# Kernel tuning notes

Measured on AMD Instinct MI355X. Metric: run time of the kernel, lower is better.

## Reference

```python
import jax, jax.numpy as jnp
import numpy as np

ENTRY_SIZE = 8192
TUPLE_SIZE = 16
N_NEURONS = ENTRY_SIZE // TUPLE_SIZE            # 512
ADDR_SPACE = 2 ** TUPLE_SIZE                     # 65536
BATCH = 4096


def setup_inputs() -> dict:
    key = jax.random.key(0)
    k1, k2, k3 = jax.random.split(key, 3)
    # Binary input bits [B, entry_size]
    inp = jax.random.randint(k1, (BATCH, ENTRY_SIZE), 0, 2, dtype=jnp.int32)
    # Permutation mapping bits -> tuples (identity permutation; arange fill)
    tuple_mapping = jnp.arange(ENTRY_SIZE, dtype=jnp.int64)
    # Dense RAM tables emulating the per-neuron dicts:
    #   counts[n, a] = number of training samples that hit address a in neuron n
    #                  (0 means the address was never trained -> not in dict)
    #   sums[n, a]   = accumulated target sum for that address
    counts = jax.random.randint(k2, (N_NEURONS, ADDR_SPACE), 0, 4, dtype=jnp.int32)
    sums = jax.random.normal(k3, (N_NEURONS, ADDR_SPACE), dtype=jnp.float32)
    return {"input": inp, "tuple_mapping": tuple_mapping, "counts": counts, "sums": sums}


def reference(input, tuple_mapping, counts, sums):
    """RegressionWisard.predict with centrality='mean'.

    input:  [B, entry_size] binary bits (int32)
    tuple_mapping: [entry_size] permutation (int)
    counts: [n_neurons, 2^tuple_size] int32 RAM hit counts
    sums:   [n_neurons, 2^tuple_size] float32 RAM target sums
    """
    B = input.shape[0]
    # Map and group bits into tuples: [B, N, T]
    mapped = jnp.take(input, tuple_mapping, axis=1).reshape(B, N_NEURONS, TUPLE_SIZE)
    # Binary address per (sample, neuron); tidx flips so bit 0 is the MSB.
    pow2 = (jnp.int32(1) << jnp.arange(TUPLE_SIZE - 1, -1, -1, dtype=jnp.int32))
    addr = jnp.einsum("bnt,t->bn", mapped, pow2)  # [B, N], values in [0, 2^T)
    neuron_idx = jnp.arange(N_NEURONS, dtype=jnp.int32)[None, :]  # [1, N]
    c = counts[neuron_idx, addr]  # [B, N]
    s = sums[neuron_idx, addr]    # [B, N]
    trained = c > 0               # dict-membership (torch.isin) equivalent
    response = jnp.sum(jnp.where(trained, s, jnp.float32(0)), axis=1)      # [B]
    counters = jnp.sum(jnp.where(trained, c, 0), axis=1).astype(s.dtype)   # [B]
    return jnp.nan_to_num(response / counters)
```

## Files before the change

kernel.cpp:

```cpp
#include <hip/hip_runtime.h>


constexpr int BATCH   = 4096;
constexpr int ENTRY   = 8192;
constexpr int TUP     = 16;
constexpr int NEUR    = ENTRY / TUP;
constexpr int LINES   = 4096;
constexpr int THREADS = 256;

typedef int v4i __attribute__((ext_vector_type(4)));

__device__ __forceinline__ int tuple_addr(
    const int* __restrict__ input, const int* __restrict__ map_n,
    int m0, bool contig, int s)
{
    if (contig) {
        const v4i* p = reinterpret_cast<const v4i*>(input + (size_t)s * ENTRY + m0);
        const v4i a0 = __builtin_nontemporal_load(p);
        const v4i a1 = __builtin_nontemporal_load(p + 1);
        const v4i a2 = __builtin_nontemporal_load(p + 2);
        const v4i a3 = __builtin_nontemporal_load(p + 3);
        return ((a0.x & 1) << 15) | ((a0.y & 1) << 14)
             | ((a0.z & 1) << 13) | ((a0.w & 1) << 12)
             | ((a1.x & 1) << 11) | ((a1.y & 1) << 10)
             | ((a1.z & 1) <<  9) | ((a1.w & 1) <<  8)
             | ((a2.x & 1) <<  7) | ((a2.y & 1) <<  6)
             | ((a2.z & 1) <<  5) | ((a2.w & 1) <<  4)
             | ((a3.x & 1) <<  3) | ((a3.y & 1) <<  2)
             | ((a3.z & 1) <<  1) |  (a3.w & 1);
    } else {
        const int* row = input + (size_t)s * ENTRY;
        int a = 0;
        #pragma unroll
        for (int t = 0; t < TUP; ++t) a = (a << 1) | (row[map_n[t]] & 1);
        return a;
    }
}

__device__ __forceinline__ int sel4(v4i v, int e01) {
    const int ab = (e01 & 1) ? v.y : v.x;
    const int cd = (e01 & 1) ? v.w : v.z;
    return (e01 & 2) ? cd : ab;
}
__device__ __forceinline__ int sel16(v4i v0, v4i v1, v4i v2, v4i v3, int e) {
    const int e2 = e & 3;
    const int a = sel4(v0, e2), b = sel4(v1, e2);
    const int c = sel4(v2, e2), d = sel4(v3, e2);
    const int ab = (e & 4) ? b : a;
    const int cd = (e & 4) ? d : c;
    return (e & 8) ? cd : ab;
}

__global__ __launch_bounds__(THREADS) void wisard_addr(
    const int* __restrict__ input,
    const int* __restrict__ mapping,
    unsigned short* __restrict__ addr_t)
{
    const int lane = threadIdx.x & 63;
    const int w    = threadIdx.x >> 6;
    const int s    = blockIdx.x * 4 + w;

    #pragma unroll 2
    for (int j = 0; j < NEUR / 64; ++j) {
        const int n = j * 64 + lane;
        const int* map_n = mapping + n * TUP;
        const int m0 = map_n[0];
        bool contig = ((m0 & 3) == 0);
        #pragma unroll
        for (int t = 1; t < TUP; ++t) contig &= (map_n[t] == m0 + t);
        const int a = tuple_addr(input, map_n, m0, contig, s);
        addr_t[(size_t)s * NEUR + n] = (unsigned short)a;
    }
}

__global__ __launch_bounds__(THREADS) void wisard_stream(
    const unsigned short* __restrict__ addr_t,
    const int*   __restrict__ counts,
    const float* __restrict__ sums,
    float2*      __restrict__ contrib)
{
    __shared__ unsigned int hist[LINES];
    __shared__ unsigned int sorted[BATCH];
    __shared__ float2 acc[BATCH];

    const int tid  = threadIdx.x;
    const int lane = tid & 63;
    const int w    = tid >> 6;
    const int n = (blockIdx.x & 7) * 64 + (blockIdx.x >> 3);

    unsigned int a[16];
    #pragma unroll
    for (int j = 0; j < 16; ++j)
        a[j] = addr_t[(size_t)(j * THREADS + tid) * NEUR + n];

    #pragma unroll
    for (int j = 0; j < LINES / THREADS; ++j) hist[j * THREADS + tid] = 0u;
    __syncthreads();
    #pragma unroll
    for (int j = 0; j < 16; ++j) atomicAdd(&hist[a[j] >> 4], 1u);
    __syncthreads();

    unsigned int* ttot = reinterpret_cast<unsigned int*>(acc);
    unsigned int* wsum = ttot + THREADS;
    unsigned int loc[16];
    unsigned int run = 0;
    #pragma unroll
    for (int j = 0; j < 16; ++j) { loc[j] = run; run += hist[tid * 16 + j]; }
    ttot[tid] = run;
    __syncthreads();
    unsigned int v = ttot[tid];
    #pragma unroll
    for (int off = 1; off < 64; off <<= 1) {
        const unsigned int u = __shfl_up(v, off, 64);
        if (lane >= off) v += u;
    }
    if (lane == 63) wsum[w] = v;
    __syncthreads();
    unsigned int woff = 0;
    for (int i = 0; i < w; ++i) woff += wsum[i];
    const unsigned int excl = woff + v - run;
    #pragma unroll
    for (int j = 0; j < 16; ++j) hist[tid * 16 + j] = excl + loc[j];
    __syncthreads();

    #pragma unroll
    for (int j = 0; j < 16; ++j) {
        const unsigned int pos = atomicAdd(&hist[a[j] >> 4], 1u);
        sorted[pos] = (a[j] << 12) | (unsigned int)(j * THREADS + tid);
    }
    __syncthreads();

    #pragma unroll
    for (int j = 0; j < 16; ++j) acc[j * THREADS + tid] = make_float2(0.0f, 0.0f);
    __syncthreads();

    const size_t tbase = (size_t)n << 16;
    for (int j = 0; j < 16; ++j) {
        const int L = j * THREADS + tid;
        const v4i* cp = reinterpret_cast<const v4i*>(counts + tbase + ((size_t)L << 4));
        const v4i* sp = reinterpret_cast<const v4i*>(
            reinterpret_cast<const int*>(sums) + tbase + ((size_t)L << 4));
        const v4i c0 = __builtin_nontemporal_load(cp);
        const v4i c1 = __builtin_nontemporal_load(cp + 1);
        const v4i c2 = __builtin_nontemporal_load(cp + 2);
        const v4i c3 = __builtin_nontemporal_load(cp + 3);
        const v4i s0 = __builtin_nontemporal_load(sp);
        const v4i s1 = __builtin_nontemporal_load(sp + 1);
        const v4i s2 = __builtin_nontemporal_load(sp + 2);
        const v4i s3 = __builtin_nontemporal_load(sp + 3);
        const unsigned int beg = (L == 0) ? 0u : hist[L - 1];
        const unsigned int end = hist[L];
        for (unsigned int k = beg; k < end; ++k) {
            const unsigned int pk = sorted[k];
            const int e  = (int)((pk >> 12) & 15u);
            const int sm = (int)(pk & 4095u);
            const int cv = sel16(c0, c1, c2, c3, e);
            const int sb = sel16(s0, s1, s2, s3, e);
            if (cv > 0) {
                float2 o;
                o.x = __int_as_float(sb);
                o.y = __int_as_float(cv);
                acc[sm] = o;
            }
        }
    }
    __syncthreads();

    #pragma unroll
    for (int j = 0; j < 16; ++j) {
        const int s = j * THREADS + tid;
        contrib[(size_t)n * BATCH + s] = acc[s];
    }
}

__global__ __launch_bounds__(THREADS) void wisard_final(
    const float2* __restrict__ contrib,
    float*        __restrict__ out)
{
    __shared__ float sr [4][64];
    __shared__ int   scn[4][64];
    const int tid  = threadIdx.x;
    const int lane = tid & 63;
    const int w    = tid >> 6;
    const int s    = blockIdx.x * 64 + lane;

    float r = 0.0f; int c = 0;
    #pragma unroll 8
    for (int i = 0; i < NEUR / 4; ++i) {
        const int n = w * (NEUR / 4) + i;
        const float2 vv = contrib[(size_t)n * BATCH + s];
        r += vv.x;
        c += __float_as_int(vv.y);
    }
    sr[w][lane] = r; scn[w][lane] = c;
    __syncthreads();
    if (w == 0) {
        r = sr[0][lane] + sr[1][lane] + sr[2][lane] + sr[3][lane];
        c = scn[0][lane] + scn[1][lane] + scn[2][lane] + scn[3][lane];
        out[s] = (c > 0) ? (r / (float)c) : 0.0f;
    }
}

__global__ __launch_bounds__(THREADS) void wisard_fallback(
    const int*   __restrict__ input,
    const int*   __restrict__ mapping,
    const int*   __restrict__ counts,
    const float* __restrict__ sums,
    float*       __restrict__ out)
{
    __shared__ float s_resp[2][THREADS / 64];
    __shared__ int   s_cnt [2][THREADS / 64];

    const int tid  = threadIdx.x;
    const int lane = tid & 63;
    const int wv   = tid >> 6;
    const int b0   = blockIdx.x * 2;

    int   cv[2][2];
    float sv[2][2];

    #pragma unroll
    for (int k = 0; k < 2; ++k) {
        const int n = tid + k * THREADS;
        const int* map_n = mapping + n * TUP;
        const int m0 = map_n[0];
        bool contig = ((m0 & 3) == 0);
        #pragma unroll
        for (int t = 1; t < TUP; ++t) contig &= (map_n[t] == m0 + t);
        #pragma unroll
        for (int s = 0; s < 2; ++s) {
            const int a = tuple_addr(input, map_n, m0, contig, b0 + s);
            const size_t idx = ((size_t)n << 16) | (unsigned)a;
            cv[s][k] = counts[idx];
            sv[s][k] = sums[idx];
        }
    }

    float resp[2]; int cnt[2];
    #pragma unroll
    for (int s = 0; s < 2; ++s) {
        resp[s] = 0.0f; cnt[s] = 0;
        #pragma unroll
        for (int k = 0; k < 2; ++k) {
            const bool t = cv[s][k] > 0;
            resp[s] += t ? sv[s][k] : 0.0f;
            cnt [s] += t ? cv[s][k] : 0;
        }
    }
    #pragma unroll
    for (int s = 0; s < 2; ++s) {
        float r = resp[s]; int c = cnt[s];
        #pragma unroll
        for (int off = 32; off > 0; off >>= 1) {
            r += __shfl_down(r, off, 64);
            c += __shfl_down(c, off, 64);
        }
        if (lane == 0) { s_resp[s][wv] = r; s_cnt[s][wv] = c; }
    }
    __syncthreads();
    if (tid < 2) {
        float r = 0.0f; int c = 0;
        #pragma unroll
        for (int w = 0; w < THREADS / 64; ++w) { r += s_resp[tid][w]; c += s_cnt[tid][w]; }
        out[b0 + tid] = (c > 0) ? (r / (float)c) : 0.0f;
    }
}

extern "C" void kernel_launch(void* const* d_in, const int* in_sizes, int n_in,
                              void* d_out, int out_size, void* d_ws, size_t ws_size,
                              hipStream_t stream) {
    (void)in_sizes; (void)n_in; (void)out_size;
    const int*   input   = (const int*)d_in[0];
    const int*   mapping = (const int*)d_in[1];
    const int*   counts  = (const int*)d_in[2];
    const float* sums    = (const float*)d_in[3];
    float*       out     = (float*)d_out;

    const size_t contrib_bytes = (size_t)NEUR * BATCH * sizeof(float2);
    const size_t addr_bytes    = (size_t)BATCH * NEUR * sizeof(unsigned short);

    if (ws_size < contrib_bytes + addr_bytes || d_ws == nullptr) {
        wisard_fallback<<<BATCH / 2, THREADS, 0, stream>>>(
            input, mapping, counts, sums, out);
        return;
    }

    float2*         contrib = (float2*)d_ws;
    unsigned short* addr_t  = (unsigned short*)((char*)d_ws + contrib_bytes);

    wisard_addr<<<BATCH / 4, THREADS, 0, stream>>>(input, mapping, addr_t);
    wisard_stream<<<NEUR, THREADS, 0, stream>>>(addr_t, counts, sums, contrib);
    wisard_final<<<BATCH / 64, THREADS, 0, stream>>>(contrib, out);
}
```

Measured before the change: 390.2 us.

## Rework wisard kernels: packed address stores, double-buffered table loads, direct contrib writes

The address kernel now handles four neurons per lane and packs four 16-bit addresses into a single 8-byte store. The stream kernel drops the shared-memory accumulator and its zeroing pass, writing each sample's contribution straight to global memory. It also double-buffers the 16-line count and sum loads so fetching the next line overlaps serving the current one. The final reduction uses 16 samples per block across 256 blocks with shuffle reductions. The risks are scattered uncoalesced global stores in the stream kernel and higher register pressure from launch bounds of 4 blocks per CU.

```diff
diff --git a/kernel.cpp b/kernel.cpp
--- a/kernel.cpp
+++ b/kernel.cpp
@@ -9,32 +9,17 @@
 constexpr int THREADS = 256;
 
 typedef int v4i __attribute__((ext_vector_type(4)));
-
-__device__ __forceinline__ int tuple_addr(
-    const int* __restrict__ input, const int* __restrict__ map_n,
-    int m0, bool contig, int s)
-{
-    if (contig) {
-        const v4i* p = reinterpret_cast<const v4i*>(input + (size_t)s * ENTRY + m0);
-        const v4i a0 = __builtin_nontemporal_load(p);
-        const v4i a1 = __builtin_nontemporal_load(p + 1);
-        const v4i a2 = __builtin_nontemporal_load(p + 2);
-        const v4i a3 = __builtin_nontemporal_load(p + 3);
-        return ((a0.x & 1) << 15) | ((a0.y & 1) << 14)
-             | ((a0.z & 1) << 13) | ((a0.w & 1) << 12)
-             | ((a1.x & 1) << 11) | ((a1.y & 1) << 10)
-             | ((a1.z & 1) <<  9) | ((a1.w & 1) <<  8)
-             | ((a2.x & 1) <<  7) | ((a2.y & 1) <<  6)
-             | ((a2.z & 1) <<  5) | ((a2.w & 1) <<  4)
-             | ((a3.x & 1) <<  3) | ((a3.y & 1) <<  2)
-             | ((a3.z & 1) <<  1) |  (a3.w & 1);
-    } else {
-        const int* row = input + (size_t)s * ENTRY;
-        int a = 0;
-        #pragma unroll
-        for (int t = 0; t < TUP; ++t) a = (a << 1) | (row[map_n[t]] & 1);
-        return a;
-    }
+typedef unsigned int uint;
+
+__device__ __forceinline__ int pack16(v4i b0, v4i b1, v4i b2, v4i b3) {
+    return ((b0.x & 1) << 15) | ((b0.y & 1) << 14)
+         | ((b0.z & 1) << 13) | ((b0.w & 1) << 12)
+         | ((b1.x & 1) << 11) | ((b1.y & 1) << 10)
+         | ((b1.z & 1) <<  9) | ((b1.w & 1) <<  8)
+         | ((b2.x & 1) <<  7) | ((b2.y & 1) <<  6)
+         | ((b2.z & 1) <<  5) | ((b2.w & 1) <<  4)
+         | ((b3.x & 1) <<  3) | ((b3.y & 1) <<  2)
+         | ((b3.z & 1) <<  1) |  (b3.w & 1);
 }
 
 __device__ __forceinline__ int sel4(v4i v, int e01) {
@@ -51,7 +36,7 @@
     return (e & 8) ? cd : ab;
 }
 
-__global__ __launch_bounds__(THREADS) void wisard_addr(
+__global__ __launch_bounds__(THREADS, 4) void wisard_addr(
     const int* __restrict__ input,
     const int* __restrict__ mapping,
     unsigned short* __restrict__ addr_t)
@@ -59,117 +44,149 @@
     const int lane = threadIdx.x & 63;
     const int w    = threadIdx.x >> 6;
     const int s    = blockIdx.x * 4 + w;
-
-    #pragma unroll 2
-    for (int j = 0; j < NEUR / 64; ++j) {
-        const int n = j * 64 + lane;
-        const int* map_n = mapping + n * TUP;
-        const int m0 = map_n[0];
-        bool contig = ((m0 & 3) == 0);
-        #pragma unroll
-        for (int t = 1; t < TUP; ++t) contig &= (map_n[t] == m0 + t);
-        const int a = tuple_addr(input, map_n, m0, contig, s);
-        addr_t[(size_t)s * NEUR + n] = (unsigned short)a;
-    }
-}
-
-__global__ __launch_bounds__(THREADS) void wisard_stream(
+    const int* row = input + (size_t)s * ENTRY;
+
+    #pragma unroll
+    for (int j = 0; j < 2; ++j) {
+        const int nb = j * 256 + lane * 4;
+        int  m0s[4];
+        bool cg [4];
+        #pragma unroll
+        for (int q = 0; q < 4; ++q) {
+            const int* map_n = mapping + (nb + q) * TUP;
+            const int m0 = map_n[0];
+            bool contig = ((m0 & 3) == 0);
+            #pragma unroll
+            for (int t = 1; t < TUP; ++t) contig &= (map_n[t] == m0 + t);
+            m0s[q] = m0; cg[q] = contig;
+        }
+
+        v4i buf[16];
+        #pragma unroll
+        for (int q = 0; q < 4; ++q) {
+            if (cg[q]) {
+                const v4i* p = reinterpret_cast<const v4i*>(row + m0s[q]);
+                buf[q * 4 + 0] = __builtin_nontemporal_load(p);
+                buf[q * 4 + 1] = __builtin_nontemporal_load(p + 1);
+                buf[q * 4 + 2] = __builtin_nontemporal_load(p + 2);
+                buf[q * 4 + 3] = __builtin_nontemporal_load(p + 3);
+            } else {
+                const int* map_n = mapping + (nb + q) * TUP;
+                #pragma unroll
+                for (int i = 0; i < 4; ++i) {
+                    v4i t;
+                    t.x = row[map_n[i * 4 + 0]];
+                    t.y = row[map_n[i * 4 + 1]];
+                    t.z = row[map_n[i * 4 + 2]];
+                    t.w = row[map_n[i * 4 + 3]];
+                    buf[q * 4 + i] = t;
+                }
+            }
+        }
+
+        const uint a0 = (uint)pack16(buf[0],  buf[1],  buf[2],  buf[3]);
+        const uint a1 = (uint)pack16(buf[4],  buf[5],  buf[6],  buf[7]);
+        const uint a2 = (uint)pack16(buf[8],  buf[9],  buf[10], buf[11]);
+        const uint a3 = (uint)pack16(buf[12], buf[13], buf[14], buf[15]);
+
+        uint2 st;
+        st.x = a0 | (a1 << 16);
+        st.y = a2 | (a3 << 16);
+        *reinterpret_cast<uint2*>(&addr_t[(size_t)s * NEUR + nb]) = st;
+    }
+}
+
+__global__ __launch_bounds__(THREADS, 4) void wisard_stream(
     const unsigned short* __restrict__ addr_t,
     const int*   __restrict__ counts,
     const float* __restrict__ sums,
     float2*      __restrict__ contrib)
 {
-    __shared__ unsigned int hist[LINES];
-    __shared__ unsigned int sorted[BATCH];
-    __shared__ float2 acc[BATCH];
+    __shared__ uint hist[LINES];
+    __shared__ uint sorted[BATCH];
+    __shared__ uint ttot[THREADS];
+    __shared__ uint wsum[4];
 
     const int tid  = threadIdx.x;
     const int lane = tid & 63;
     const int w    = tid >> 6;
     const int n = (blockIdx.x & 7) * 64 + (blockIdx.x >> 3);
 
-    unsigned int a[16];
+    uint a[16];
     #pragma unroll
     for (int j = 0; j < 16; ++j)
         a[j] = addr_t[(size_t)(j * THREADS + tid) * NEUR + n];
 
     #pragma unroll
-    for (int j = 0; j < LINES / THREADS; ++j) hist[j * THREADS + tid] = 0u;
+    for (int j = 0; j < 16; ++j) hist[j * THREADS + tid] = 0u;
     __syncthreads();
     #pragma unroll
     for (int j = 0; j < 16; ++j) atomicAdd(&hist[a[j] >> 4], 1u);
     __syncthreads();
 
-    unsigned int* ttot = reinterpret_cast<unsigned int*>(acc);
-    unsigned int* wsum = ttot + THREADS;
-    unsigned int loc[16];
-    unsigned int run = 0;
+    uint loc[16];
+    uint run = 0;
     #pragma unroll
     for (int j = 0; j < 16; ++j) { loc[j] = run; run += hist[tid * 16 + j]; }
     ttot[tid] = run;
     __syncthreads();
-    unsigned int v = ttot[tid];
+    uint v = ttot[tid];
     #pragma unroll
     for (int off = 1; off < 64; off <<= 1) {
-        const unsigned int u = __shfl_up(v, off, 64);
+        const uint u = __shfl_up(v, off, 64);
         if (lane >= off) v += u;
     }
     if (lane == 63) wsum[w] = v;
     __syncthreads();
-    unsigned int woff = 0;
+    uint woff = 0;
     for (int i = 0; i < w; ++i) woff += wsum[i];
-    const unsigned int excl = woff + v - run;
+    const uint excl = woff + v - run;
     #pragma unroll
     for (int j = 0; j < 16; ++j) hist[tid * 16 + j] = excl + loc[j];
     __syncthreads();
 
     #pragma unroll
     for (int j = 0; j < 16; ++j) {
-        const unsigned int pos = atomicAdd(&hist[a[j] >> 4], 1u);
-        sorted[pos] = (a[j] << 12) | (unsigned int)(j * THREADS + tid);
-    }
-    __syncthreads();
-
-    #pragma unroll
-    for (int j = 0; j < 16; ++j) acc[j * THREADS + tid] = make_float2(0.0f, 0.0f);
-    __syncthreads();
-
-    const size_t tbase = (size_t)n << 16;
-    for (int j = 0; j < 16; ++j) {
-        const int L = j * THREADS + tid;
-        const v4i* cp = reinterpret_cast<const v4i*>(counts + tbase + ((size_t)L << 4));
-        const v4i* sp = reinterpret_cast<const v4i*>(
-            reinterpret_cast<const int*>(sums) + tbase + ((size_t)L << 4));
-        const v4i c0 = __builtin_nontemporal_load(cp);
-        const v4i c1 = __builtin_nontemporal_load(cp + 1);
-        const v4i c2 = __builtin_nontemporal_load(cp + 2);
-        const v4i c3 = __builtin_nontemporal_load(cp + 3);
-        const v4i s0 = __builtin_nontemporal_load(sp);
-        const v4i s1 = __builtin_nontemporal_load(sp + 1);
-        const v4i s2 = __builtin_nontemporal_load(sp + 2);
-        const v4i s3 = __builtin_nontemporal_load(sp + 3);
-        const unsigned int beg = (L == 0) ? 0u : hist[L - 1];
-        const unsigned int end = hist[L];
-        for (unsigned int k = beg; k < end; ++k) {
-            const unsigned int pk = sorted[k];
+        const uint pos = atomicAdd(&hist[a[j] >> 4], 1u);
+        sorted[pos] = (a[j] << 12) | (uint)(j * THREADS + tid);
+    }
+    __syncthreads();
+
+    const int* ci = counts + ((size_t)n << 16);
+    const int* si = reinterpret_cast<const int*>(sums) + ((size_t)n << 16);
+    float2*    cb = contrib + (size_t)n * BATCH;
+
+    auto LD = [&](int L, v4i* c, v4i* s4) {
+        const v4i* cp = reinterpret_cast<const v4i*>(ci + ((size_t)L << 4));
+        const v4i* sp = reinterpret_cast<const v4i*>(si + ((size_t)L << 4));
+        c[0] = cp[0]; c[1] = cp[1]; c[2] = cp[2]; c[3] = cp[3];
+        s4[0] = sp[0]; s4[1] = sp[1]; s4[2] = sp[2]; s4[3] = sp[3];
+    };
+    auto SERVE = [&](int L, const v4i* c, const v4i* s4) {
+        const uint beg = (L == 0) ? 0u : hist[L - 1];
+        const uint end = hist[L];
+        for (uint k = beg; k < end; ++k) {
+            const uint pk = sorted[k];
             const int e  = (int)((pk >> 12) & 15u);
             const int sm = (int)(pk & 4095u);
-            const int cv = sel16(c0, c1, c2, c3, e);
-            const int sb = sel16(s0, s1, s2, s3, e);
-            if (cv > 0) {
-                float2 o;
-                o.x = __int_as_float(sb);
-                o.y = __int_as_float(cv);
-                acc[sm] = o;
-            }
-        }
-    }
-    __syncthreads();
-
-    #pragma unroll
-    for (int j = 0; j < 16; ++j) {
-        const int s = j * THREADS + tid;
-        contrib[(size_t)n * BATCH + s] = acc[s];
+            const int cv = sel16(c[0], c[1], c[2], c[3], e);
+            const int sb = sel16(s4[0], s4[1], s4[2], s4[3], e);
+            const bool tr = cv > 0;
+            float2 o;
+            o.x = tr ? __int_as_float(sb) : 0.0f;
+            o.y = __int_as_float(tr ? cv : 0);
+            cb[sm] = o;
+        }
+    };
+
+    v4i cA[4], sA[4], cB[4], sB[4];
+    LD(tid, cA, sA);
+    #pragma unroll
+    for (int j = 0; j < 16; j += 2) {
+        LD((j + 1) * THREADS + tid, cB, sB);
+        SERVE(j * THREADS + tid, cA, sA);
+        if (j + 2 < 16) LD((j + 2) * THREADS + tid, cA, sA);
+        SERVE((j + 1) * THREADS + tid, cB, sB);
     }
 }
 
@@ -177,27 +194,31 @@
     const float2* __restrict__ contrib,
     float*        __restrict__ out)
 {
-    __shared__ float sr [4][64];
-    __shared__ int   scn[4][64];
+    __shared__ float sr [4][16];
+    __shared__ int   scn[4][16];
     const int tid  = threadIdx.x;
     const int lane = tid & 63;
     const int w    = tid >> 6;
-    const int s    = blockIdx.x * 64 + lane;
+    const int sloc = tid & 15;
+    const int g    = tid >> 4;
+    const int s    = blockIdx.x * 16 + sloc;
 
     float r = 0.0f; int c = 0;
     #pragma unroll 8
-    for (int i = 0; i < NEUR / 4; ++i) {
-        const int n = w * (NEUR / 4) + i;
+    for (int i = 0; i < NEUR / 16; ++i) {
+        const int n = g + i * 16;
         const float2 vv = contrib[(size_t)n * BATCH + s];
         r += vv.x;
         c += __float_as_int(vv.y);
     }
-    sr[w][lane] = r; scn[w][lane] = c;
-    __syncthreads();
-    if (w == 0) {
-        r = sr[0][lane] + sr[1][lane] + sr[2][lane] + sr[3][lane];
-        c = scn[0][lane] + scn[1][lane] + scn[2][lane] + scn[3][lane];
-        out[s] = (c > 0) ? (r / (float)c) : 0.0f;
+    r += __shfl_down(r, 32, 64); c += __shfl_down(c, 32, 64);
+    r += __shfl_down(r, 16, 64); c += __shfl_down(c, 16, 64);
+    if (lane < 16) { sr[w][lane] = r; scn[w][lane] = c; }
+    __syncthreads();
+    if (tid < 16) {
+        r = sr[0][tid] + sr[1][tid] + sr[2][tid] + sr[3][tid];
+        c = scn[0][tid] + scn[1][tid] + scn[2][tid] + scn[3][tid];
+        out[blockIdx.x * 16 + tid] = (c > 0) ? (r / (float)c) : 0.0f;
     }
 }
 
@@ -229,7 +250,19 @@
         for (int t = 1; t < TUP; ++t) contig &= (map_n[t] == m0 + t);
         #pragma unroll
         for (int s = 0; s < 2; ++s) {
-            const int a = tuple_addr(input, map_n, m0, contig, b0 + s);
+            const int* row = input + (size_t)(b0 + s) * ENTRY;
+            int a;
+            if (contig) {
+                const v4i* p = reinterpret_cast<const v4i*>(row + m0);
+                a = pack16(__builtin_nontemporal_load(p),
+                           __builtin_nontemporal_load(p + 1),
+                           __builtin_nontemporal_load(p + 2),
+                           __builtin_nontemporal_load(p + 3));
+            } else {
+                a = 0;
+                #pragma unroll
+                for (int t = 0; t < TUP; ++t) a = (a << 1) | (row[map_n[t]] & 1);
+            }
             const size_t idx = ((size_t)n << 16) | (unsigned)a;
             cv[s][k] = counts[idx];
             sv[s][k] = sums[idx];
@@ -290,5 +323,5 @@
 
     wisard_addr<<<BATCH / 4, THREADS, 0, stream>>>(input, mapping, addr_t);
     wisard_stream<<<NEUR, THREADS, 0, stream>>>(addr_t, counts, sums, contrib);
-    wisard_final<<<BATCH / 64, THREADS, 0, stream>>>(contrib, out);
-}
+    wisard_final<<<BATCH / 16, THREADS, 0, stream>>>(contrib, out);
+}
```

Measured after the change: 439.3 us. +12.6%, slower.
